# Kernel optimization log

Hardware: AMD Instinct MI355X
Metric: run time of the kernel (lower is better)

Reference implementation:

```python
import jax, jax.numpy as jnp
import numpy as np

HALF_PI = np.float32(np.pi / 2.0)
EPS = 1e-8

def feature_map(x):
    # [B, L] -> [B, L, 2]: standard quantum-inspired embedding
    return jnp.stack([jnp.cos(HALF_PI * x), jnp.sin(HALF_PI * x)], axis=-1)

def setup_inputs() -> dict:
    key = jax.random.key(0)
    k1, k2, k3, k4 = jax.random.split(key, 4)
    B, L, F, D, C = 32768, 256, 2, 32, 10
    x = jax.random.uniform(k1, (B, L), dtype=jnp.float32)
    core0 = jax.random.normal(k2, (F, 1, D), dtype=jnp.float32) * 0.1
    cores_mid = jax.random.normal(k3, (L - 2, F, D, D), dtype=jnp.float32) * 0.1
    coreN = jax.random.normal(k4, (F, D, C), dtype=jnp.float32) * 0.1
    return {"x": x, "core0": core0, "cores_mid": cores_mid, "coreN": coreN}

def reference(x, core0, cores_mid, coreN):
    feats = feature_map(x)                      # [B, L, F]
    # first site: M = v0 @ A0  -> [B, D]
    M0 = jnp.einsum('bf,fd->bd', feats[:, 0, :], core0[:, 0, :])

    # sequential scan over middle sites with per-step L2 normalization
    vs = jnp.transpose(feats[:, 1:-1, :], (1, 0, 2))  # [L-2, B, F]

    def step(M, inputs):
        v, A = inputs                           # v: [B,F], A: [F,D,D]
        M = jnp.einsum('ba,bf,fac->bc', M, v, A)
        M = M / (jnp.linalg.norm(M, axis=1, keepdims=True) + EPS)
        return M, None

    M, _ = jax.lax.scan(step, M0, (vs, cores_mid))

    # last site and readout
    final = jnp.einsum('bf,fac->bac', feats[:, -1, :], coreN)  # [B, D, C]
    logits = jnp.einsum('ba,bac->bc', M, final)                # [B, C]
    return logits
```

## Files before the change

### kernel.cpp

```cpp
#include <hip/hip_runtime.h>
#include <hip/hip_bf16.h>

#define B_TOTAL   32768
#define L_SITES   256
#define N_MID     254
#define HALF_PI_F 1.57079632679489662f
#define EPS_NORM  1e-8f

#define WS_FRAG 0
#define WS_C0   520192
#define WS_CN   520256

typedef short bf16x8 __attribute__((ext_vector_type(8)));
typedef float f32x4  __attribute__((ext_vector_type(4)));

__device__ __host__ __forceinline__ int pi_perm(int quad, int j) {
    return (j < 4) ? (quad * 4 + j) : (16 + quad * 4 + (j - 4));
}

__device__ __forceinline__ unsigned short f2bf(float f) {
    unsigned u = __builtin_bit_cast(unsigned, f);
    u += 0x7FFFu + ((u >> 16) & 1u);
    return (unsigned short)(u >> 16);
}
__device__ __forceinline__ float bf2f(unsigned short h) {
    unsigned u = ((unsigned)h) << 16;
    return __builtin_bit_cast(float, u);
}
__device__ __forceinline__ bf16x8 asbf(uint4 u) {
    return __builtin_bit_cast(bf16x8, u);
}
__device__ __forceinline__ void psincos(float x, float* s, float* c) {
    float u = x * x;
    float sp = fmaf(u, -3.5988432352121e-6f, 1.6044118478736e-4f);
    sp = fmaf(u, sp, -4.6817541353187e-3f);
    sp = fmaf(u, sp, 7.9692626246167e-2f);
    sp = fmaf(u, sp, -6.4596409750625e-1f);
    sp = fmaf(u, sp, 1.5707963267949f);
    *s = x * sp;
    float cp = fmaf(u, 4.7108749076366e-7f, -2.5202042373061e-5f);
    cp = fmaf(u, cp, 9.1926027483943e-4f);
    cp = fmaf(u, cp, -2.0863480763353e-2f);
    cp = fmaf(u, cp, 2.5366950790105e-1f);
    cp = fmaf(u, cp, -1.2337005501362f);
    *c = fmaf(u, cp, 1.0f);
}
__device__ __forceinline__ unsigned pkbf2(float a, float b) {
    float2 p; p.x = a; p.y = b;
    __hip_bfloat162 h2 = __float22bfloat162_rn(p);
    unsigned u;
    __builtin_memcpy(&u, &h2, 4);
    return u;
}
__device__ __forceinline__ void split8(const float* v, bf16x8& hi, bf16x8& lo) {
    uint4 H, L;
    unsigned* hp = (unsigned*)&H;
    unsigned* lp = (unsigned*)&L;
    #pragma unroll
    for (int d = 0; d < 4; ++d) {
        float a = v[2 * d], b = v[2 * d + 1];
        unsigned hb = pkbf2(a, b);
        float h0 = __builtin_bit_cast(float, hb << 16);
        float h1 = __builtin_bit_cast(float, hb & 0xFFFF0000u);
        hp[d] = hb;
        lp[d] = pkbf2(a - h0, b - h1);
    }
    hi = __builtin_bit_cast(bf16x8, H);
    lo = __builtin_bit_cast(bf16x8, L);
}
__device__ __forceinline__ bool detect_bf16(const unsigned* x_raw, int lane) {
    unsigned v = x_raw[lane];
    return __ballot((v & 0xFFFFu) >= 0x4000u) == 0ull;
}
__device__ __forceinline__ float ldx(bool bf, const void* x, int b, int site) {
    if (bf) return bf2f(((const unsigned short*)x)[(size_t)b * L_SITES + site]);
    return ((const float*)x)[(size_t)b * L_SITES + site];
}

__global__ __launch_bounds__(256)
void aux_all(const void* __restrict__ x_in, const void* __restrict__ c0_in,
             const void* __restrict__ am_in, const void* __restrict__ cn_in,
             float* __restrict__ ws) {
    const int lane = threadIdx.x & 63;
    const bool bf = detect_bf16((const unsigned*)x_in, lane);
    const int b = blockIdx.x;

    if (b < N_MID) {
        const int t = b;
        __shared__ float amS[2][32][33];
        if (!bf) {
            const float* src = (const float*)am_in + (size_t)t * 2048;
            for (int idx = threadIdx.x; idx < 2048; idx += 256) {
                amS[idx >> 10][(idx >> 5) & 31][idx & 31] = src[idx];
            }
        } else {
            const unsigned short* src = (const unsigned short*)am_in + (size_t)t * 2048;
            for (int idx = threadIdx.x; idx < 2048; idx += 256) {
                amS[idx >> 10][(idx >> 5) & 31][idx & 31] = bf2f(src[idx]);
            }
        }
        __syncthreads();
        #pragma unroll
        for (int u = 0; u < 2; ++u) {
            const int oi = threadIdx.x + 256 * u;
            const int q  = oi >> 6;
            const int l  = oi & 63;
            const int h  = q >> 2;
            const int kh = (q >> 1) & 1;
            const int p  = q & 1;
            const int m  = h * 16 + (l & 15);
            const int kb = (l >> 4) * 8;
            unsigned dw[4];
            #pragma unroll
            for (int d = 0; d < 4; ++d) {
                unsigned e01[2];
                #pragma unroll
                for (int s = 0; s < 2; ++s) {
                    int k = kb + 2 * d + s;
                    int a = pi_perm(k >> 3, k & 7);
                    float v = amS[kh][a][m];
                    unsigned short hi = f2bf(v);
                    e01[s] = (p == 0) ? hi : f2bf(v - bf2f(hi));
                }
                dw[d] = e01[0] | (e01[1] << 16);
            }
            uint4 o; o.x = dw[0]; o.y = dw[1]; o.z = dw[2]; o.w = dw[3];
            ((uint4*)ws)[(size_t)(t * 8 + q) * 64 + l] = o;
        }
    } else {
        for (int i = threadIdx.x; i < 640; i += 256) {
            if (i < 64)
                ws[WS_C0 + i] = bf ? bf2f(((const unsigned short*)c0_in)[i])
                                   : ((const float*)c0_in)[i];
            ws[WS_CN + i] = bf ? bf2f(((const unsigned short*)cn_in)[i])
                               : ((const float*)cn_in)[i];
        }
    }
}

__global__ __launch_bounds__(256, 2)
void mps_mfma(const float* __restrict__ ws, const void* __restrict__ x_in,
              void* __restrict__ out) {
    const int lane = threadIdx.x & 63;
    const int w    = threadIdx.x >> 6;
    const int r    = lane & 15;
    const int quad = lane >> 4;
    const int b0   = (blockIdx.x * 4 + w) * 16;
    const uint4* __restrict__ BF = (const uint4*)ws;
    const int i = b0 + r;
    const bool bf = detect_bf16((const unsigned*)x_in, lane);

    float mm[8];
    {
        float x0 = ldx(bf, x_in, i, 0);
        float sn, cs; psincos(x0, &sn, &cs);
        const float* c0 = ws + WS_C0;
        #pragma unroll
        for (int j = 0; j < 8; ++j) {
            int a = pi_perm(quad, j);
            mm[j] = cs * c0[a] + sn * c0[32 + a];
        }
    }
    float ct, st;
    { float xc = ldx(bf, x_in, i, 1); psincos(xc, &st, &ct); }
    float xn = ldx(bf, x_in, i, 2);

    #pragma unroll 1
    for (int t = 0; t < N_MID; ++t) {
        const uint4* F = BF + (size_t)t * 512 + lane;
        uint4 f0 = F[0];    uint4 f1 = F[64];
        uint4 f2 = F[128];  uint4 f3 = F[192];
        uint4 f4 = F[256];  uint4 f5 = F[320];
        uint4 f6 = F[384];  uint4 f7 = F[448];

        float ctn, stn; psincos(xn, &stn, &ctn);
        int xr = t + 3; if (xr > 255) xr = 255;
        float xn2 = ldx(bf, x_in, i, xr);

        bf16x8 mh, ml;
        split8(mm, mh, ml);
        const f32x4 z = {0.f, 0.f, 0.f, 0.f};
        __builtin_amdgcn_s_setprio(1);
        f32x4 a00 = __builtin_amdgcn_mfma_f32_16x16x32_bf16(asbf(f0), mh, z, 0, 0, 0);
        f32x4 a01 = __builtin_amdgcn_mfma_f32_16x16x32_bf16(asbf(f2), mh, z, 0, 0, 0);
        f32x4 a10 = __builtin_amdgcn_mfma_f32_16x16x32_bf16(asbf(f4), mh, z, 0, 0, 0);
        f32x4 a11 = __builtin_amdgcn_mfma_f32_16x16x32_bf16(asbf(f6), mh, z, 0, 0, 0);
        f32x4 b00 = __builtin_amdgcn_mfma_f32_16x16x32_bf16(asbf(f1), mh, z, 0, 0, 0);
        f32x4 b01 = __builtin_amdgcn_mfma_f32_16x16x32_bf16(asbf(f3), mh, z, 0, 0, 0);
        f32x4 b10 = __builtin_amdgcn_mfma_f32_16x16x32_bf16(asbf(f5), mh, z, 0, 0, 0);
        f32x4 b11 = __builtin_amdgcn_mfma_f32_16x16x32_bf16(asbf(f7), mh, z, 0, 0, 0);
        f32x4 c00 = __builtin_amdgcn_mfma_f32_16x16x32_bf16(asbf(f0), ml, z, 0, 0, 0);
        f32x4 c01 = __builtin_amdgcn_mfma_f32_16x16x32_bf16(asbf(f2), ml, z, 0, 0, 0);
        f32x4 c10 = __builtin_amdgcn_mfma_f32_16x16x32_bf16(asbf(f4), ml, z, 0, 0, 0);
        f32x4 c11 = __builtin_amdgcn_mfma_f32_16x16x32_bf16(asbf(f6), ml, z, 0, 0, 0);
        __builtin_amdgcn_s_setprio(0);
        #pragma unroll
        for (int j = 0; j < 4; ++j) {
            float p00 = (a00[j] + b00[j]) + c00[j];
            float p01 = (a01[j] + b01[j]) + c01[j];
            float p10 = (a10[j] + b10[j]) + c10[j];
            float p11 = (a11[j] + b11[j]) + c11[j];
            mm[j]     = fmaf(st, p01, ct * p00);
            mm[4 + j] = fmaf(st, p11, ct * p10);
        }

        if (((t & 7) == 7) || (t == N_MID - 1)) {
            float ss = 0.f;
            #pragma unroll
            for (int j = 0; j < 8; ++j) ss = fmaf(mm[j], mm[j], ss);
            ss += __shfl_xor(ss, 16);
            ss += __shfl_xor(ss, 32);
            float kk = 1.0f / (sqrtf(ss) + EPS_NORM);
            #pragma unroll
            for (int j = 0; j < 8; ++j) mm[j] *= kk;
        }

        ct = ctn; st = stn; xn = xn2;
    }

    {
        float xN = ldx(bf, x_in, i, L_SITES - 1);
        float sN, cN; psincos(xN, &sN, &cN);
        const float* kn = ws + WS_CN;
        float acc[10];
        #pragma unroll
        for (int c = 0; c < 10; ++c) acc[c] = 0.f;
        #pragma unroll
        for (int j = 0; j < 8; ++j) {
            int a = pi_perm(quad, j);
            float Ma = mm[j];
            #pragma unroll
            for (int c = 0; c < 10; ++c) {
                float fin = cN * kn[a * 10 + c] + sN * kn[320 + a * 10 + c];
                acc[c] = fmaf(Ma, fin, acc[c]);
            }
        }
        #pragma unroll
        for (int c = 0; c < 10; ++c) {
            acc[c] += __shfl_xor(acc[c], 16);
            acc[c] += __shfl_xor(acc[c], 32);
        }
        if (quad == 0) {
            if (bf) {
                __hip_bfloat16* o = (__hip_bfloat16*)out;
                #pragma unroll
                for (int c = 0; c < 10; ++c)
                    o[(size_t)(b0 + r) * 10 + c] = __float2bfloat16(acc[c]);
            } else {
                float* o = (float*)out;
                #pragma unroll
                for (int c = 0; c < 10; ++c)
                    o[(size_t)(b0 + r) * 10 + c] = acc[c];
            }
        }
    }
}

extern "C" void kernel_launch(void* const* d_in, const int* in_sizes, int n_in,
                              void* d_out, int out_size, void* d_ws, size_t ws_size,
                              hipStream_t stream) {
    float* ws = (float*)d_ws;
    aux_all<<<N_MID + 1, 256, 0, stream>>>(d_in[0], d_in[1], d_in[2], d_in[3], ws);
    mps_mfma<<<512, 256, 0, stream>>>(ws, d_in[0], d_out);
}
```

Baseline: 250.9 us.

## Stage x rows in shared memory, chain MFMA accumulators, split aux blocks

```diff
diff --git a/kernel.cpp b/kernel.cpp
--- a/kernel.cpp
+++ b/kernel.cpp
@@ -72,10 +72,6 @@
     unsigned v = x_raw[lane];
     return __ballot((v & 0xFFFFu) >= 0x4000u) == 0ull;
 }
-__device__ __forceinline__ float ldx(bool bf, const void* x, int b, int site) {
-    if (bf) return bf2f(((const unsigned short*)x)[(size_t)b * L_SITES + site]);
-    return ((const float*)x)[(size_t)b * L_SITES + site];
-}
 
 __global__ __launch_bounds__(256)
 void aux_all(const void* __restrict__ x_in, const void* __restrict__ c0_in,
@@ -85,48 +81,44 @@
     const bool bf = detect_bf16((const unsigned*)x_in, lane);
     const int b = blockIdx.x;
 
-    if (b < N_MID) {
-        const int t = b;
-        __shared__ float amS[2][32][33];
+    if (b < 2 * N_MID) {
+        const int t  = b >> 1;
+        const int kh = b & 1;
+        __shared__ float amS[32][33];
         if (!bf) {
-            const float* src = (const float*)am_in + (size_t)t * 2048;
-            for (int idx = threadIdx.x; idx < 2048; idx += 256) {
-                amS[idx >> 10][(idx >> 5) & 31][idx & 31] = src[idx];
+            const float* src = (const float*)am_in + (size_t)t * 2048 + kh * 1024;
+            for (int idx = threadIdx.x; idx < 1024; idx += 256)
+                amS[idx >> 5][idx & 31] = src[idx];
+        } else {
+            const unsigned short* src =
+                (const unsigned short*)am_in + (size_t)t * 2048 + kh * 1024;
+            for (int idx = threadIdx.x; idx < 1024; idx += 256)
+                amS[idx >> 5][idx & 31] = bf2f(src[idx]);
+        }
+        __syncthreads();
+        const int l  = threadIdx.x & 63;
+        const int qi = threadIdx.x >> 6;
+        const int h  = qi >> 1;
+        const int p  = qi & 1;
+        const int q  = h * 4 + kh * 2 + p;
+        const int m  = h * 16 + (l & 15);
+        const int kb = (l >> 4) * 8;
+        unsigned dw[4];
+        #pragma unroll
+        for (int d = 0; d < 4; ++d) {
+            unsigned e01[2];
+            #pragma unroll
+            for (int s = 0; s < 2; ++s) {
+                int k = kb + 2 * d + s;
+                int a = pi_perm(k >> 3, k & 7);
+                float v = amS[a][m];
+                unsigned short hi = f2bf(v);
+                e01[s] = (p == 0) ? hi : f2bf(v - bf2f(hi));
             }
-        } else {
-            const unsigned short* src = (const unsigned short*)am_in + (size_t)t * 2048;
-            for (int idx = threadIdx.x; idx < 2048; idx += 256) {
-                amS[idx >> 10][(idx >> 5) & 31][idx & 31] = bf2f(src[idx]);
-            }
-        }
-        __syncthreads();
-        #pragma unroll
-        for (int u = 0; u < 2; ++u) {
-            const int oi = threadIdx.x + 256 * u;
-            const int q  = oi >> 6;
-            const int l  = oi & 63;
-            const int h  = q >> 2;
-            const int kh = (q >> 1) & 1;
-            const int p  = q & 1;
-            const int m  = h * 16 + (l & 15);
-            const int kb = (l >> 4) * 8;
-            unsigned dw[4];
-            #pragma unroll
-            for (int d = 0; d < 4; ++d) {
-                unsigned e01[2];
-                #pragma unroll
-                for (int s = 0; s < 2; ++s) {
-                    int k = kb + 2 * d + s;
-                    int a = pi_perm(k >> 3, k & 7);
-                    float v = amS[kh][a][m];
-                    unsigned short hi = f2bf(v);
-                    e01[s] = (p == 0) ? hi : f2bf(v - bf2f(hi));
-                }
-                dw[d] = e01[0] | (e01[1] << 16);
-            }
-            uint4 o; o.x = dw[0]; o.y = dw[1]; o.z = dw[2]; o.w = dw[3];
-            ((uint4*)ws)[(size_t)(t * 8 + q) * 64 + l] = o;
-        }
+            dw[d] = e01[0] | (e01[1] << 16);
+        }
+        uint4 o; o.x = dw[0]; o.y = dw[1]; o.z = dw[2]; o.w = dw[3];
+        ((uint4*)ws)[(size_t)(t * 8 + q) * 64 + l] = o;
     } else {
         for (int i = threadIdx.x; i < 640; i += 256) {
             if (i < 64)
@@ -141,18 +133,48 @@
 __global__ __launch_bounds__(256, 2)
 void mps_mfma(const float* __restrict__ ws, const void* __restrict__ x_in,
               void* __restrict__ out) {
+    __shared__ float xs[L_SITES][64];
     const int lane = threadIdx.x & 63;
     const int w    = threadIdx.x >> 6;
     const int r    = lane & 15;
     const int quad = lane >> 4;
-    const int b0   = (blockIdx.x * 4 + w) * 16;
+    const int bb   = blockIdx.x * 64;
+    const int bl   = w * 16 + r;
+    const int b0   = bb + w * 16;
     const uint4* __restrict__ BF = (const uint4*)ws;
-    const int i = b0 + r;
     const bool bf = detect_bf16((const unsigned*)x_in, lane);
+
+    if (!bf) {
+        const float4* x4 = (const float4*)x_in;
+        const int row = threadIdx.x >> 2;
+        const int q   = threadIdx.x & 3;
+        #pragma unroll
+        for (int u = 0; u < 16; ++u) {
+            int c4 = q + u * 4;
+            float4 v = x4[(size_t)(bb + row) * (L_SITES / 4) + c4];
+            xs[c4 * 4 + 0][row] = v.x;
+            xs[c4 * 4 + 1][row] = v.y;
+            xs[c4 * 4 + 2][row] = v.z;
+            xs[c4 * 4 + 3][row] = v.w;
+        }
+    } else {
+        const uint4* x8 = (const uint4*)x_in;
+        const int row = threadIdx.x >> 2;
+        const int q   = threadIdx.x & 3;
+        #pragma unroll
+        for (int u = 0; u < 8; ++u) {
+            int c8 = q + u * 4;
+            uint4 v = x8[(size_t)(bb + row) * (L_SITES / 8) + c8];
+            const unsigned short* e = (const unsigned short*)&v;
+            #pragma unroll
+            for (int k = 0; k < 8; ++k) xs[c8 * 8 + k][row] = bf2f(e[k]);
+        }
+    }
+    __syncthreads();
 
     float mm[8];
     {
-        float x0 = ldx(bf, x_in, i, 0);
+        float x0 = xs[0][bl];
         float sn, cs; psincos(x0, &sn, &cs);
         const float* c0 = ws + WS_C0;
         #pragma unroll
@@ -162,8 +184,8 @@
         }
     }
     float ct, st;
-    { float xc = ldx(bf, x_in, i, 1); psincos(xc, &st, &ct); }
-    float xn = ldx(bf, x_in, i, 2);
+    psincos(xs[1][bl], &st, &ct);
+    float xn = xs[2][bl];
 
     #pragma unroll 1
     for (int t = 0; t < N_MID; ++t) {
@@ -175,33 +197,29 @@
 
         float ctn, stn; psincos(xn, &stn, &ctn);
         int xr = t + 3; if (xr > 255) xr = 255;
-        float xn2 = ldx(bf, x_in, i, xr);
+        float xn2 = xs[xr][bl];
 
         bf16x8 mh, ml;
         split8(mm, mh, ml);
         const f32x4 z = {0.f, 0.f, 0.f, 0.f};
         __builtin_amdgcn_s_setprio(1);
-        f32x4 a00 = __builtin_amdgcn_mfma_f32_16x16x32_bf16(asbf(f0), mh, z, 0, 0, 0);
-        f32x4 a01 = __builtin_amdgcn_mfma_f32_16x16x32_bf16(asbf(f2), mh, z, 0, 0, 0);
-        f32x4 a10 = __builtin_amdgcn_mfma_f32_16x16x32_bf16(asbf(f4), mh, z, 0, 0, 0);
-        f32x4 a11 = __builtin_amdgcn_mfma_f32_16x16x32_bf16(asbf(f6), mh, z, 0, 0, 0);
-        f32x4 b00 = __builtin_amdgcn_mfma_f32_16x16x32_bf16(asbf(f1), mh, z, 0, 0, 0);
-        f32x4 b01 = __builtin_amdgcn_mfma_f32_16x16x32_bf16(asbf(f3), mh, z, 0, 0, 0);
-        f32x4 b10 = __builtin_amdgcn_mfma_f32_16x16x32_bf16(asbf(f5), mh, z, 0, 0, 0);
-        f32x4 b11 = __builtin_amdgcn_mfma_f32_16x16x32_bf16(asbf(f7), mh, z, 0, 0, 0);
-        f32x4 c00 = __builtin_amdgcn_mfma_f32_16x16x32_bf16(asbf(f0), ml, z, 0, 0, 0);
-        f32x4 c01 = __builtin_amdgcn_mfma_f32_16x16x32_bf16(asbf(f2), ml, z, 0, 0, 0);
-        f32x4 c10 = __builtin_amdgcn_mfma_f32_16x16x32_bf16(asbf(f4), ml, z, 0, 0, 0);
-        f32x4 c11 = __builtin_amdgcn_mfma_f32_16x16x32_bf16(asbf(f6), ml, z, 0, 0, 0);
+        f32x4 p00 = __builtin_amdgcn_mfma_f32_16x16x32_bf16(asbf(f0), mh, z, 0, 0, 0);
+        f32x4 p01 = __builtin_amdgcn_mfma_f32_16x16x32_bf16(asbf(f2), mh, z, 0, 0, 0);
+        f32x4 p10 = __builtin_amdgcn_mfma_f32_16x16x32_bf16(asbf(f4), mh, z, 0, 0, 0);
+        f32x4 p11 = __builtin_amdgcn_mfma_f32_16x16x32_bf16(asbf(f6), mh, z, 0, 0, 0);
+        p00 = __builtin_amdgcn_mfma_f32_16x16x32_bf16(asbf(f1), mh, p00, 0, 0, 0);
+        p01 = __builtin_amdgcn_mfma_f32_16x16x32_bf16(asbf(f3), mh, p01, 0, 0, 0);
+        p10 = __builtin_amdgcn_mfma_f32_16x16x32_bf16(asbf(f5), mh, p10, 0, 0, 0);
+        p11 = __builtin_amdgcn_mfma_f32_16x16x32_bf16(asbf(f7), mh, p11, 0, 0, 0);
+        p00 = __builtin_amdgcn_mfma_f32_16x16x32_bf16(asbf(f0), ml, p00, 0, 0, 0);
+        p01 = __builtin_amdgcn_mfma_f32_16x16x32_bf16(asbf(f2), ml, p01, 0, 0, 0);
+        p10 = __builtin_amdgcn_mfma_f32_16x16x32_bf16(asbf(f4), ml, p10, 0, 0, 0);
+        p11 = __builtin_amdgcn_mfma_f32_16x16x32_bf16(asbf(f6), ml, p11, 0, 0, 0);
         __builtin_amdgcn_s_setprio(0);
         #pragma unroll
         for (int j = 0; j < 4; ++j) {
-            float p00 = (a00[j] + b00[j]) + c00[j];
-            float p01 = (a01[j] + b01[j]) + c01[j];
-            float p10 = (a10[j] + b10[j]) + c10[j];
-            float p11 = (a11[j] + b11[j]) + c11[j];
-            mm[j]     = fmaf(st, p01, ct * p00);
-            mm[4 + j] = fmaf(st, p11, ct * p10);
+            mm[j]     = fmaf(st, p01[j], ct * p00[j]);
+            mm[4 + j] = fmaf(st, p11[j], ct * p10[j]);
         }
 
         if (((t & 7) == 7) || (t == N_MID - 1)) {
@@ -219,7 +237,7 @@
     }
 
     {
-        float xN = ldx(bf, x_in, i, L_SITES - 1);
+        float xN = xs[L_SITES - 1][bl];
         float sN, cN; psincos(xN, &sN, &cN);
         const float* kn = ws + WS_CN;
         float acc[10];
@@ -260,6 +278,6 @@
                               void* d_out, int out_size, void* d_ws, size_t ws_size,
                               hipStream_t stream) {
     float* ws = (float*)d_ws;
-    aux_all<<<N_MID + 1, 256, 0, stream>>>(d_in[0], d_in[1], d_in[2], d_in[3], ws);
+    aux_all<<<2 * N_MID + 1, 256, 0, stream>>>(d_in[0], d_in[1], d_in[2], d_in[3], ws);
     mps_mfma<<<512, 256, 0, stream>>>(ws, d_in[0], d_out);
 }
```

Measured after the change: 219.8 us. -12.4%, faster.
